# Kernel optimization log

Hardware: AMD Instinct MI355X
Metric: run time of the kernel (lower is better)

The kernel has to match this reference:

```python
import jax, jax.numpy as jnp
import numpy as np

VOCAB, T, E, H, O, B = 401, 140, 128, 256, 3, 4096


def setup_inputs() -> dict:
    key = jax.random.key(0)
    ks = jax.random.split(key, 8)
    s_e = 1.0 / np.sqrt(H)
    return {
        "input": jax.random.randint(ks[0], (B, T), 0, VOCAB),
        "hidden": jnp.zeros((B, H), dtype=jnp.float32),
        "embed": jax.random.normal(ks[1], (VOCAB, E), dtype=jnp.float32),
        "W_ih": jax.random.uniform(ks[2], (3 * H, E), jnp.float32, -s_e, s_e),
        "W_hh": jax.random.uniform(ks[3], (3 * H, H), jnp.float32, -s_e, s_e),
        "b_ih": jax.random.uniform(ks[4], (3 * H,), jnp.float32, -s_e, s_e),
        "b_hh": jax.random.uniform(ks[5], (3 * H,), jnp.float32, -s_e, s_e),
        "W_out": jax.random.uniform(ks[6], (O, H), jnp.float32, -s_e, s_e),
        "b_out": jax.random.uniform(ks[7], (O,), jnp.float32, -s_e, s_e),
    }


def reference(input, hidden, embed, W_ih, W_hh, b_ih, b_hh, W_out, b_out):
    # Embedding lookup: [B, T, E]
    x = embed[input]
    # Precompute input-side gate projections for all timesteps: [B, T, 3H]
    gi = jnp.einsum("bte,ge->btg", x, W_ih) + b_ih

    def step(h, gi_t):
        gh = h @ W_hh.T + b_hh  # [B, 3H]
        i_r, i_z, i_n = jnp.split(gi_t, 3, axis=-1)
        h_r, h_z, h_n = jnp.split(gh, 3, axis=-1)
        r = jax.nn.sigmoid(i_r + h_r)
        z = jax.nn.sigmoid(i_z + h_z)
        n = jnp.tanh(i_n + r * h_n)
        h_new = (1.0 - z) * n + z * h
        return h_new, None

    h_final, _ = jax.lax.scan(step, hidden, jnp.swapaxes(gi, 0, 1))
    logits = h_final @ W_out.T + b_out  # [B, O]
    return jax.nn.log_softmax(logits, axis=1), h_final
```

## Files before the change

kernel.cpp:

```cpp
#include <hip/hip_runtime.h>

typedef __attribute__((ext_vector_type(8))) short short8;
typedef __attribute__((ext_vector_type(4))) float f32x4;
typedef unsigned short ushort_t;
typedef unsigned int uint_t;

#define VOCAB 401
#define T_ 140
#define E_ 128
#define H_ 256
#define B_ 4096
#define HPAD 264

__device__ float Gf[VOCAB * 768];
__device__ ushort_t WhhB[768 * H_];

__device__ __forceinline__ float bf2f(ushort_t u) {
  union { uint_t i; float f; } x; x.i = ((uint_t)u) << 16; return x.f;
}
__device__ __forceinline__ ushort_t f2bf(float f) {
  union { float f; uint_t i; } x; x.f = f;
  uint_t r = x.i + 0x7FFFu + ((x.i >> 16) & 1u);
  return (ushort_t)(r >> 16);
}
__device__ __forceinline__ float fast_sigmoid(float x) {
  return __builtin_amdgcn_rcpf(1.f + __builtin_amdgcn_exp2f(-1.442695041f * x));
}
__device__ __forceinline__ float fast_tanh(float x) {
  return 1.f - 2.f * __builtin_amdgcn_rcpf(1.f + __builtin_amdgcn_exp2f(2.885390082f * x));
}
__device__ __forceinline__ float ldf(const void* p, size_t i, int isb) {
  return isb ? bf2f(((const ushort_t*)p)[i]) : ((const float*)p)[i];
}
__device__ __forceinline__ void ld8f(const void* p, size_t idx, int isb, float* o) {
  if (isb) {
    short8 v = *(const short8*)((const ushort_t*)p + idx);
#pragma unroll
    for (int e = 0; e < 8; ++e) o[e] = bf2f((ushort_t)v[e]);
  } else {
    f32x4 a = *(const f32x4*)((const float*)p + idx);
    f32x4 b = *(const f32x4*)((const float*)p + idx + 4);
#pragma unroll
    for (int e = 0; e < 4; ++e) { o[e] = a[e]; o[4 + e] = b[e]; }
  }
}
__device__ __forceinline__ int block_probe_isbf16(const ushort_t* embed_raw, int* s) {
  if (threadIdx.x < 64) {
    ushort_t v = embed_raw[2 * threadIdx.x];
    int e = (v >> 7) & 0xFF;
    unsigned long long m = __ballot(e >= 100 && e <= 140);
    if (threadIdx.x == 0) *s = (__popcll(m) >= 40) ? 1 : 0;
  }
  __syncthreads();
  return *s;
}

__global__ void canon_whh(const void* __restrict__ W_hh, const ushort_t* __restrict__ embed_raw) {
  __shared__ int sISB;
  int isb = block_probe_isbf16(embed_raw, &sISB);
  int i4 = (blockIdx.x * 256 + threadIdx.x) * 4;
  if (isb) {
    *(uint2*)&WhhB[i4] = *(const uint2*)((const ushort_t*)W_hh + i4);
  } else {
    f32x4 v = *(const f32x4*)((const float*)W_hh + i4);
    uint2 pk;
    pk.x = (uint_t)f2bf(v[0]) | ((uint_t)f2bf(v[1]) << 16);
    pk.y = (uint_t)f2bf(v[2]) | ((uint_t)f2bf(v[3]) << 16);
    *(uint2*)&WhhB[i4] = pk;
  }
}

__global__ void build_G(const void* __restrict__ embed,
                        const void* __restrict__ W_ih,
                        const void* __restrict__ b_ih,
                        const void* __restrict__ b_hh) {
  __shared__ float emb[E_];
  __shared__ int sISB;
  const int isb = block_probe_isbf16((const ushort_t*)embed, &sISB);
  const int v = blockIdx.x, g = blockIdx.y, j = threadIdx.x;
  if (j < E_) emb[j] = ldf(embed, (size_t)v * E_ + j, isb);
  __syncthreads();
  const int row = g * H_ + j;
  float s = 0.f;
#pragma unroll
  for (int k8 = 0; k8 < E_ / 8; ++k8) {
    float wv[8];
    ld8f(W_ih, (size_t)row * E_ + k8 * 8, isb, wv);
#pragma unroll
    for (int e = 0; e < 8; ++e) s += emb[k8 * 8 + e] * wv[e];
  }
  s += ldf(b_ih, row, isb);
  if (g < 2) s += ldf(b_hh, row, isb);
  Gf[v * 768 + row] = s;
}

__launch_bounds__(1024)
__global__ void gru_persist(const int* __restrict__ input,
                            const void* __restrict__ hidden,
                            const void* __restrict__ b_hh,
                            const void* __restrict__ W_out,
                            const void* __restrict__ b_out,
                            const ushort_t* __restrict__ embed_raw,
                            void* __restrict__ out) {
  __shared__ ushort_t hB[2][16 * HPAD];
  __shared__ float bhhn[H_];
  __shared__ int ids[16 * T_];
  __shared__ int sISB;

  const int isb  = block_probe_isbf16(embed_raw, &sISB);
  const int tid  = threadIdx.x;
  const int w    = tid >> 6;
  const int lane = tid & 63;
  const int quad = lane >> 4;
  const int col  = lane & 15;
  const int wg   = blockIdx.x;
  const int u0   = w << 4;
  const int u0q  = u0 + (quad << 2);

  if (tid < 512) {
    int r = tid >> 5, c0 = (tid & 31) << 3;
    size_t gi = (size_t)(wg * 16 + r) * H_ + c0;
    ushort_t* dst = &hB[0][r * HPAD + c0];
    if (isb) {
      *(short8*)dst = *(const short8*)((const ushort_t*)hidden + gi);
    } else {
      float tmp[8];
      ld8f(hidden, gi, 0, tmp);
#pragma unroll
      for (int e = 0; e < 8; ++e) dst[e] = f2bf(tmp[e]);
    }
  }
  if (tid < H_) bhhn[tid] = ldf(b_hh, 512 + tid, isb);
  for (int k = tid; k < 16 * T_; k += 1024)
    ids[k] = input[(size_t)wg * 16 * T_ + k] * 3072;

  short8 wA[3][8];
#pragma unroll
  for (int g = 0; g < 3; ++g) {
    const ushort_t* wrow = WhhB + (size_t)(g * H_ + u0 + col) * H_ + (quad << 3);
#pragma unroll
    for (int kt = 0; kt < 8; ++kt) wA[g][kt] = *(const short8*)(wrow + kt * 32);
  }

  __syncthreads();

  float hreg[4];
#pragma unroll
  for (int i = 0; i < 4; ++i)
    hreg[i] = bf2f(hB[0][col * HPAD + u0q + i]);

  const int idbase = col * T_;
  const char* gB = (const char*)Gf + (size_t)u0q * 4;

  f32x4 accr, accz, gin;
  {
    int goff = ids[idbase];
    accr = *(const f32x4*)(gB + goff);
    accz = *(const f32x4*)(gB + goff + H_ * 4);
    gin  = *(const f32x4*)(gB + goff + 2 * H_ * 4);
  }

  for (int t = 0; t < T_; ++t) {
    const int cur = t & 1;
    const int nxt = cur ^ 1;
    const ushort_t* hr = &hB[cur][col * HPAD + (quad << 3)];

    f32x4 an = {0.f, 0.f, 0.f, 0.f};
#pragma unroll
    for (int kt = 0; kt < 8; ++kt) {
      short8 b = *(const short8*)(hr + kt * 32);
      accr = __builtin_amdgcn_mfma_f32_16x16x32_bf16(wA[0][kt], b, accr, 0, 0, 0);
      accz = __builtin_amdgcn_mfma_f32_16x16x32_bf16(wA[1][kt], b, accz, 0, 0, 0);
      an   = __builtin_amdgcn_mfma_f32_16x16x32_bf16(wA[2][kt], b, an,   0, 0, 0);
    }

    int tn = t + 1; if (tn == T_) tn = 0;
    int goff2 = ids[idbase + tn];

    f32x4 bh = *(const f32x4*)&bhhn[u0q];

    uint_t rr[4];
#pragma unroll
    for (int i = 0; i < 4; ++i) {
      float r_ = fast_sigmoid(accr[i]);
      float z_ = fast_sigmoid(accz[i]);
      float hn = an[i] + bh[i];
      float n  = fast_tanh(gin[i] + r_ * hn);
      float h  = n + z_ * (hreg[i] - n);
      hreg[i] = h;
      union { float f; uint_t u; } c; c.f = h;
      rr[i] = c.u + 0x7FFFu + ((c.u >> 16) & 1u);
    }
    ushort_t* hw = &hB[nxt][col * HPAD + u0q];
    *(uint_t*)&hw[0] = __builtin_amdgcn_perm(rr[1], rr[0], 0x07060302);
    *(uint_t*)&hw[2] = __builtin_amdgcn_perm(rr[3], rr[2], 0x07060302);

    accr = *(const f32x4*)(gB + goff2);
    accz = *(const f32x4*)(gB + goff2 + H_ * 4);
    gin  = *(const f32x4*)(gB + goff2 + 2 * H_ * 4);

    __syncthreads();
  }

  {
    const ushort_t* hrow = &hB[0][w * HPAD + (lane << 2)];
    float h0 = bf2f(hrow[0]), h1 = bf2f(hrow[1]), h2 = bf2f(hrow[2]), h3 = bf2f(hrow[3]);
    float d[3];
#pragma unroll
    for (int o = 0; o < 3; ++o) {
      size_t base = (size_t)o * H_ + (lane << 2);
      d[o] = ldf(W_out, base, isb) * h0 + ldf(W_out, base + 1, isb) * h1 +
             ldf(W_out, base + 2, isb) * h2 + ldf(W_out, base + 3, isb) * h3;
      for (int off = 1; off < 64; off <<= 1) d[o] += __shfl_xor(d[o], off);
    }
    if (lane == 0) {
      float l0 = d[0] + ldf(b_out, 0, isb);
      float l1 = d[1] + ldf(b_out, 1, isb);
      float l2 = d[2] + ldf(b_out, 2, isb);
      float m = fmaxf(l0, fmaxf(l1, l2));
      float s = __builtin_amdgcn_exp2f((l0 - m) * 1.442695041f) +
                __builtin_amdgcn_exp2f((l1 - m) * 1.442695041f) +
                __builtin_amdgcn_exp2f((l2 - m) * 1.442695041f);
      float ls = __builtin_amdgcn_logf(s) * 0.6931471806f;
      size_t ob = (size_t)(wg * 16 + w) * 3;
      float o0 = l0 - m - ls, o1 = l1 - m - ls, o2 = l2 - m - ls;
      if (isb) {
        ushort_t* ob16 = (ushort_t*)out;
        ob16[ob] = f2bf(o0); ob16[ob + 1] = f2bf(o1); ob16[ob + 2] = f2bf(o2);
      } else {
        float* of = (float*)out;
        of[ob] = o0; of[ob + 1] = o1; of[ob + 2] = o2;
      }
    }
  }
  {
    int e = tid << 2;
    int bb = e >> 8, uu = e & 255;
    const ushort_t* src = &hB[0][bb * HPAD + uu];
    size_t oi = 12288 + (size_t)wg * 4096 + e;
    if (isb) {
      *(uint2*)((ushort_t*)out + oi) = *(const uint2*)src;
    } else {
      float* of = (float*)out;
      of[oi] = bf2f(src[0]); of[oi + 1] = bf2f(src[1]);
      of[oi + 2] = bf2f(src[2]); of[oi + 3] = bf2f(src[3]);
    }
  }
}

extern "C" void kernel_launch(void* const* d_in, const int* in_sizes, int n_in,
                              void* d_out, int out_size, void* d_ws, size_t ws_size,
                              hipStream_t stream) {
  (void)in_sizes; (void)n_in; (void)out_size; (void)d_ws; (void)ws_size;
  const int* input = (const int*)d_in[0];
  const void* hidden = d_in[1];
  const void* embed  = d_in[2];
  const void* W_ih   = d_in[3];
  const void* W_hh   = d_in[4];
  const void* b_hh   = d_in[6];
  const void* W_out  = d_in[7];
  const void* b_out  = d_in[8];
  const void* b_ih   = d_in[5];

  canon_whh<<<192, 256, 0, stream>>>(W_hh, (const ushort_t*)embed);
  build_G<<<dim3(VOCAB, 3), 256, 0, stream>>>(embed, W_ih, b_ih, b_hh);
  gru_persist<<<B_ / 16, 1024, 0, stream>>>(input, hidden, b_hh, W_out, b_out,
                                            (const ushort_t*)embed, d_out);
}
```

Baseline: 435.0 us.

## Halve GRU block to 512 threads with two row-tiles per wave

The persistent GRU kernel now runs 8 waves per block, each owning two 16-unit tiles, so weight fragments double per wave. Launch bounds allow two blocks per CU. The n-gate bias is folded into the MFMA accumulator init and the id table is padded to drop the wrap branch. build_G now processes 8 vocab rows per block, reusing each W_ih load across 8 embeddings. Register pressure rises (wA holds 48 short8), which risks spills or lower occupancy.

```diff
diff --git a/kernel.cpp b/kernel.cpp
--- a/kernel.cpp
+++ b/kernel.cpp
@@ -74,27 +74,39 @@
                         const void* __restrict__ W_ih,
                         const void* __restrict__ b_ih,
                         const void* __restrict__ b_hh) {
-  __shared__ float emb[E_];
+  __shared__ float emb[8][E_];
   __shared__ int sISB;
   const int isb = block_probe_isbf16((const ushort_t*)embed, &sISB);
-  const int v = blockIdx.x, g = blockIdx.y, j = threadIdx.x;
-  if (j < E_) emb[j] = ldf(embed, (size_t)v * E_ + j, isb);
+  const int vb = blockIdx.x;
+  const int g  = blockIdx.y;
+  const int j  = threadIdx.x;
+  for (int idx = j; idx < 8 * E_; idx += 256) {
+    int s = idx >> 7, e = idx & 127;
+    int v = vb * 8 + s; if (v > VOCAB - 1) v = VOCAB - 1;
+    emb[s][e] = ldf(embed, (size_t)v * E_ + e, isb);
+  }
   __syncthreads();
   const int row = g * H_ + j;
-  float s = 0.f;
-#pragma unroll
+  float acc[8];
+#pragma unroll
+  for (int s = 0; s < 8; ++s) acc[s] = 0.f;
   for (int k8 = 0; k8 < E_ / 8; ++k8) {
     float wv[8];
     ld8f(W_ih, (size_t)row * E_ + k8 * 8, isb, wv);
 #pragma unroll
-    for (int e = 0; e < 8; ++e) s += emb[k8 * 8 + e] * wv[e];
-  }
-  s += ldf(b_ih, row, isb);
-  if (g < 2) s += ldf(b_hh, row, isb);
-  Gf[v * 768 + row] = s;
-}
-
-__launch_bounds__(1024)
+    for (int s = 0; s < 8; ++s)
+#pragma unroll
+      for (int e = 0; e < 8; ++e) acc[s] += emb[s][k8 * 8 + e] * wv[e];
+  }
+  float bias = ldf(b_ih, row, isb) + ((g < 2) ? ldf(b_hh, row, isb) : 0.f);
+#pragma unroll
+  for (int s = 0; s < 8; ++s) {
+    int v = vb * 8 + s;
+    if (v < VOCAB) Gf[v * 768 + row] = acc[s] + bias;
+  }
+}
+
+__launch_bounds__(512, 2)
 __global__ void gru_persist(const int* __restrict__ input,
                             const void* __restrict__ hidden,
                             const void* __restrict__ b_hh,
@@ -104,7 +116,7 @@
                             void* __restrict__ out) {
   __shared__ ushort_t hB[2][16 * HPAD];
   __shared__ float bhhn[H_];
-  __shared__ int ids[16 * T_];
+  __shared__ int ids[16 * (T_ + 1)];
   __shared__ int sISB;
 
   const int isb  = block_probe_isbf16(embed_raw, &sISB);
@@ -114,10 +126,11 @@
   const int quad = lane >> 4;
   const int col  = lane & 15;
   const int wg   = blockIdx.x;
-  const int u0   = w << 4;
-  const int u0q  = u0 + (quad << 2);
-
-  if (tid < 512) {
+  const int u0   = w << 5;
+  const int u0q0 = u0 + (quad << 2);
+  const int u0q1 = u0 + 16 + (quad << 2);
+
+  {
     int r = tid >> 5, c0 = (tid & 31) << 3;
     size_t gi = (size_t)(wg * 16 + r) * H_ + c0;
     ushort_t* dst = &hB[0][r * HPAD + c0];
@@ -131,79 +144,114 @@
     }
   }
   if (tid < H_) bhhn[tid] = ldf(b_hh, 512 + tid, isb);
-  for (int k = tid; k < 16 * T_; k += 1024)
-    ids[k] = input[(size_t)wg * 16 * T_ + k] * 3072;
-
-  short8 wA[3][8];
-#pragma unroll
-  for (int g = 0; g < 3; ++g) {
-    const ushort_t* wrow = WhhB + (size_t)(g * H_ + u0 + col) * H_ + (quad << 3);
-#pragma unroll
-    for (int kt = 0; kt < 8; ++kt) wA[g][kt] = *(const short8*)(wrow + kt * 32);
-  }
+  for (int k = tid; k < 16 * (T_ + 1); k += 512) {
+    int b = k / (T_ + 1), t = k - b * (T_ + 1);
+    ids[k] = (t < T_) ? input[(size_t)wg * 16 * T_ + b * T_ + t] * 3072 : 0;
+  }
+
+  short8 wA[3][2][8];
+#pragma unroll
+  for (int g = 0; g < 3; ++g)
+#pragma unroll
+    for (int tl = 0; tl < 2; ++tl) {
+      const ushort_t* wrow = WhhB + (size_t)(g * H_ + u0 + tl * 16 + col) * H_ + (quad << 3);
+#pragma unroll
+      for (int kt = 0; kt < 8; ++kt) wA[g][tl][kt] = *(const short8*)(wrow + kt * 32);
+    }
 
   __syncthreads();
 
-  float hreg[4];
-#pragma unroll
-  for (int i = 0; i < 4; ++i)
-    hreg[i] = bf2f(hB[0][col * HPAD + u0q + i]);
-
-  const int idbase = col * T_;
-  const char* gB = (const char*)Gf + (size_t)u0q * 4;
-
-  f32x4 accr, accz, gin;
+  float hreg0[4], hreg1[4];
+#pragma unroll
+  for (int i = 0; i < 4; ++i) {
+    hreg0[i] = bf2f(hB[0][col * HPAD + u0q0 + i]);
+    hreg1[i] = bf2f(hB[0][col * HPAD + u0q1 + i]);
+  }
+  const f32x4 bh0 = *(const f32x4*)&bhhn[u0q0];
+  const f32x4 bh1 = *(const f32x4*)&bhhn[u0q1];
+
+  const int idbase = col * (T_ + 1);
+  const char* gB = (const char*)Gf + (size_t)u0q0 * 4;
+
+  f32x4 a0r, a0z, g0n, a1r, a1z, g1n;
   {
     int goff = ids[idbase];
-    accr = *(const f32x4*)(gB + goff);
-    accz = *(const f32x4*)(gB + goff + H_ * 4);
-    gin  = *(const f32x4*)(gB + goff + 2 * H_ * 4);
-  }
-
+    a0r = *(const f32x4*)(gB + goff);
+    a0z = *(const f32x4*)(gB + goff + 1024);
+    g0n = *(const f32x4*)(gB + goff + 2048);
+    a1r = *(const f32x4*)(gB + goff + 64);
+    a1z = *(const f32x4*)(gB + goff + 1024 + 64);
+    g1n = *(const f32x4*)(gB + goff + 2048 + 64);
+  }
+
+#pragma unroll 2
   for (int t = 0; t < T_; ++t) {
     const int cur = t & 1;
     const int nxt = cur ^ 1;
     const ushort_t* hr = &hB[cur][col * HPAD + (quad << 3)];
-
-    f32x4 an = {0.f, 0.f, 0.f, 0.f};
+    const int goff_n = ids[idbase + t + 1];
+
+    f32x4 a0n = bh0;
 #pragma unroll
     for (int kt = 0; kt < 8; ++kt) {
       short8 b = *(const short8*)(hr + kt * 32);
-      accr = __builtin_amdgcn_mfma_f32_16x16x32_bf16(wA[0][kt], b, accr, 0, 0, 0);
-      accz = __builtin_amdgcn_mfma_f32_16x16x32_bf16(wA[1][kt], b, accz, 0, 0, 0);
-      an   = __builtin_amdgcn_mfma_f32_16x16x32_bf16(wA[2][kt], b, an,   0, 0, 0);
-    }
-
-    int tn = t + 1; if (tn == T_) tn = 0;
-    int goff2 = ids[idbase + tn];
-
-    f32x4 bh = *(const f32x4*)&bhhn[u0q];
-
-    uint_t rr[4];
-#pragma unroll
-    for (int i = 0; i < 4; ++i) {
-      float r_ = fast_sigmoid(accr[i]);
-      float z_ = fast_sigmoid(accz[i]);
-      float hn = an[i] + bh[i];
-      float n  = fast_tanh(gin[i] + r_ * hn);
-      float h  = n + z_ * (hreg[i] - n);
-      hreg[i] = h;
-      union { float f; uint_t u; } c; c.f = h;
-      rr[i] = c.u + 0x7FFFu + ((c.u >> 16) & 1u);
-    }
-    ushort_t* hw = &hB[nxt][col * HPAD + u0q];
-    *(uint_t*)&hw[0] = __builtin_amdgcn_perm(rr[1], rr[0], 0x07060302);
-    *(uint_t*)&hw[2] = __builtin_amdgcn_perm(rr[3], rr[2], 0x07060302);
-
-    accr = *(const f32x4*)(gB + goff2);
-    accz = *(const f32x4*)(gB + goff2 + H_ * 4);
-    gin  = *(const f32x4*)(gB + goff2 + 2 * H_ * 4);
+      a0r = __builtin_amdgcn_mfma_f32_16x16x32_bf16(wA[0][0][kt], b, a0r, 0, 0, 0);
+      a0z = __builtin_amdgcn_mfma_f32_16x16x32_bf16(wA[1][0][kt], b, a0z, 0, 0, 0);
+      a0n = __builtin_amdgcn_mfma_f32_16x16x32_bf16(wA[2][0][kt], b, a0n, 0, 0, 0);
+    }
+    {
+      uint_t rr[4];
+#pragma unroll
+      for (int i = 0; i < 4; ++i) {
+        float r_ = fast_sigmoid(a0r[i]);
+        float z_ = fast_sigmoid(a0z[i]);
+        float n  = fast_tanh(g0n[i] + r_ * a0n[i]);
+        float h  = n + z_ * (hreg0[i] - n);
+        hreg0[i] = h;
+        union { float f; uint_t u; } c; c.f = h;
+        rr[i] = c.u + 0x7FFFu + ((c.u >> 16) & 1u);
+      }
+      ushort_t* hw = &hB[nxt][col * HPAD + u0q0];
+      *(uint_t*)&hw[0] = __builtin_amdgcn_perm(rr[1], rr[0], 0x07060302);
+      *(uint_t*)&hw[2] = __builtin_amdgcn_perm(rr[3], rr[2], 0x07060302);
+    }
+    a0r = *(const f32x4*)(gB + goff_n);
+    a0z = *(const f32x4*)(gB + goff_n + 1024);
+    g0n = *(const f32x4*)(gB + goff_n + 2048);
+
+    f32x4 a1n = bh1;
+#pragma unroll
+    for (int kt = 0; kt < 8; ++kt) {
+      short8 b = *(const short8*)(hr + kt * 32);
+      a1r = __builtin_amdgcn_mfma_f32_16x16x32_bf16(wA[0][1][kt], b, a1r, 0, 0, 0);
+      a1z = __builtin_amdgcn_mfma_f32_16x16x32_bf16(wA[1][1][kt], b, a1z, 0, 0, 0);
+      a1n = __builtin_amdgcn_mfma_f32_16x16x32_bf16(wA[2][1][kt], b, a1n, 0, 0, 0);
+    }
+    {
+      uint_t rr[4];
+#pragma unroll
+      for (int i = 0; i < 4; ++i) {
+        float r_ = fast_sigmoid(a1r[i]);
+        float z_ = fast_sigmoid(a1z[i]);
+        float n  = fast_tanh(g1n[i] + r_ * a1n[i]);
+        float h  = n + z_ * (hreg1[i] - n);
+        hreg1[i] = h;
+        union { float f; uint_t u; } c; c.f = h;
+        rr[i] = c.u + 0x7FFFu + ((c.u >> 16) & 1u);
+      }
+      ushort_t* hw = &hB[nxt][col * HPAD + u0q1];
+      *(uint_t*)&hw[0] = __builtin_amdgcn_perm(rr[1], rr[0], 0x07060302);
+      *(uint_t*)&hw[2] = __builtin_amdgcn_perm(rr[3], rr[2], 0x07060302);
+    }
+    a1r = *(const f32x4*)(gB + goff_n + 64);
+    a1z = *(const f32x4*)(gB + goff_n + 1024 + 64);
+    g1n = *(const f32x4*)(gB + goff_n + 2048 + 64);
 
     __syncthreads();
   }
 
-  {
-    const ushort_t* hrow = &hB[0][w * HPAD + (lane << 2)];
+  for (int rb = w; rb < 16; rb += 8) {
+    const ushort_t* hrow = &hB[0][rb * HPAD + (lane << 2)];
     float h0 = bf2f(hrow[0]), h1 = bf2f(hrow[1]), h2 = bf2f(hrow[2]), h3 = bf2f(hrow[3]);
     float d[3];
 #pragma unroll
@@ -222,7 +270,7 @@
                 __builtin_amdgcn_exp2f((l1 - m) * 1.442695041f) +
                 __builtin_amdgcn_exp2f((l2 - m) * 1.442695041f);
       float ls = __builtin_amdgcn_logf(s) * 0.6931471806f;
-      size_t ob = (size_t)(wg * 16 + w) * 3;
+      size_t ob = (size_t)(wg * 16 + rb) * 3;
       float o0 = l0 - m - ls, o1 = l1 - m - ls, o2 = l2 - m - ls;
       if (isb) {
         ushort_t* ob16 = (ushort_t*)out;
@@ -234,16 +282,16 @@
     }
   }
   {
-    int e = tid << 2;
+    int e = tid << 3;
     int bb = e >> 8, uu = e & 255;
     const ushort_t* src = &hB[0][bb * HPAD + uu];
     size_t oi = 12288 + (size_t)wg * 4096 + e;
     if (isb) {
-      *(uint2*)((ushort_t*)out + oi) = *(const uint2*)src;
+      *(short8*)((ushort_t*)out + oi) = *(const short8*)src;
     } else {
       float* of = (float*)out;
-      of[oi] = bf2f(src[0]); of[oi + 1] = bf2f(src[1]);
-      of[oi + 2] = bf2f(src[2]); of[oi + 3] = bf2f(src[3]);
+#pragma unroll
+      for (int q = 0; q < 8; ++q) of[oi + q] = bf2f(src[q]);
     }
   }
 }
@@ -257,13 +305,13 @@
   const void* embed  = d_in[2];
   const void* W_ih   = d_in[3];
   const void* W_hh   = d_in[4];
+  const void* b_ih   = d_in[5];
   const void* b_hh   = d_in[6];
   const void* W_out  = d_in[7];
   const void* b_out  = d_in[8];
-  const void* b_ih   = d_in[5];
 
   canon_whh<<<192, 256, 0, stream>>>(W_hh, (const ushort_t*)embed);
-  build_G<<<dim3(VOCAB, 3), 256, 0, stream>>>(embed, W_ih, b_ih, b_hh);
-  gru_persist<<<B_ / 16, 1024, 0, stream>>>(input, hidden, b_hh, W_out, b_out,
-                                            (const ushort_t*)embed, d_out);
-}
+  build_G<<<dim3(51, 3), 256, 0, stream>>>(embed, W_ih, b_ih, b_hh);
+  gru_persist<<<B_ / 16, 512, 0, stream>>>(input, hidden, b_hh, W_out, b_out,
+                                           (const ushort_t*)embed, d_out);
+}
```

Measured after the change: 443.7 us. +2.0%, slower.

## Merge prep kernels, interleave sigmoid with n-gate MFMAs, use raw barrier

Applied to the files above, without the earlier changes.

The two setup kernels become one launch. The input-projection table build now handles 8 vocab rows per block, so each W_ih load is reused across those rows. In the recurrent loop, the n-gate MFMA chain now runs after r/z, with the sigmoid math interleaved and b_hh_n folded into the accumulator init. The ids table gets a padded sentinel column so the next-step index needs no wrap check, and __syncthreads is replaced by an explicit lgkmcnt wait plus s_barrier. The aim is to hide the transcendental latency behind matrix work and cut per-step sync and launch overhead, at the cost of relying on hand-placed barrier semantics.

```diff
diff --git a/kernel.cpp b/kernel.cpp
--- a/kernel.cpp
+++ b/kernel.cpp
@@ -55,43 +55,57 @@
   return *s;
 }
 
-__global__ void canon_whh(const void* __restrict__ W_hh, const ushort_t* __restrict__ embed_raw) {
-  __shared__ int sISB;
-  int isb = block_probe_isbf16(embed_raw, &sISB);
-  int i4 = (blockIdx.x * 256 + threadIdx.x) * 4;
-  if (isb) {
-    *(uint2*)&WhhB[i4] = *(const uint2*)((const ushort_t*)W_hh + i4);
-  } else {
-    f32x4 v = *(const f32x4*)((const float*)W_hh + i4);
-    uint2 pk;
-    pk.x = (uint_t)f2bf(v[0]) | ((uint_t)f2bf(v[1]) << 16);
-    pk.y = (uint_t)f2bf(v[2]) | ((uint_t)f2bf(v[3]) << 16);
-    *(uint2*)&WhhB[i4] = pk;
-  }
-}
-
-__global__ void build_G(const void* __restrict__ embed,
-                        const void* __restrict__ W_ih,
-                        const void* __restrict__ b_ih,
-                        const void* __restrict__ b_hh) {
-  __shared__ float emb[E_];
+__global__ void prep(const void* __restrict__ W_hh,
+                     const void* __restrict__ embed,
+                     const void* __restrict__ W_ih,
+                     const void* __restrict__ b_ih,
+                     const void* __restrict__ b_hh) {
+  __shared__ float emb[8][E_];
   __shared__ int sISB;
   const int isb = block_probe_isbf16((const ushort_t*)embed, &sISB);
-  const int v = blockIdx.x, g = blockIdx.y, j = threadIdx.x;
-  if (j < E_) emb[j] = ldf(embed, (size_t)v * E_ + j, isb);
+  const int bid = blockIdx.x;
+  const int j = threadIdx.x;
+
+  if (bid >= 153) {
+    int i4 = ((bid - 153) * 256 + j) * 4;
+    if (isb) {
+      *(uint2*)&WhhB[i4] = *(const uint2*)((const ushort_t*)W_hh + i4);
+    } else {
+      f32x4 v = *(const f32x4*)((const float*)W_hh + i4);
+      uint2 pk;
+      pk.x = (uint_t)f2bf(v[0]) | ((uint_t)f2bf(v[1]) << 16);
+      pk.y = (uint_t)f2bf(v[2]) | ((uint_t)f2bf(v[3]) << 16);
+      *(uint2*)&WhhB[i4] = pk;
+    }
+    return;
+  }
+
+  const int vb = bid / 3;
+  const int g  = bid - vb * 3;
+  for (int idx = j; idx < 8 * E_; idx += 256) {
+    int s = idx >> 7, e = idx & 127;
+    int v = vb * 8 + s; if (v > VOCAB - 1) v = VOCAB - 1;
+    emb[s][e] = ldf(embed, (size_t)v * E_ + e, isb);
+  }
   __syncthreads();
   const int row = g * H_ + j;
-  float s = 0.f;
-#pragma unroll
+  float acc[8];
+#pragma unroll
+  for (int s = 0; s < 8; ++s) acc[s] = 0.f;
   for (int k8 = 0; k8 < E_ / 8; ++k8) {
     float wv[8];
     ld8f(W_ih, (size_t)row * E_ + k8 * 8, isb, wv);
 #pragma unroll
-    for (int e = 0; e < 8; ++e) s += emb[k8 * 8 + e] * wv[e];
-  }
-  s += ldf(b_ih, row, isb);
-  if (g < 2) s += ldf(b_hh, row, isb);
-  Gf[v * 768 + row] = s;
+    for (int s = 0; s < 8; ++s)
+#pragma unroll
+      for (int e = 0; e < 8; ++e) acc[s] += emb[s][k8 * 8 + e] * wv[e];
+  }
+  float bias = ldf(b_ih, row, isb) + ((g < 2) ? ldf(b_hh, row, isb) : 0.f);
+#pragma unroll
+  for (int s = 0; s < 8; ++s) {
+    int v = vb * 8 + s;
+    if (v < VOCAB) Gf[v * 768 + row] = acc[s] + bias;
+  }
 }
 
 __launch_bounds__(1024)
@@ -104,7 +118,7 @@
                             void* __restrict__ out) {
   __shared__ ushort_t hB[2][16 * HPAD];
   __shared__ float bhhn[H_];
-  __shared__ int ids[16 * T_];
+  __shared__ int ids[16 * (T_ + 1)];
   __shared__ int sISB;
 
   const int isb  = block_probe_isbf16(embed_raw, &sISB);
@@ -131,8 +145,10 @@
     }
   }
   if (tid < H_) bhhn[tid] = ldf(b_hh, 512 + tid, isb);
-  for (int k = tid; k < 16 * T_; k += 1024)
-    ids[k] = input[(size_t)wg * 16 * T_ + k] * 3072;
+  for (int k = tid; k < 16 * (T_ + 1); k += 1024) {
+    int b = k / (T_ + 1), t = k - b * (T_ + 1);
+    ids[k] = (t < T_) ? input[(size_t)wg * 16 * T_ + b * T_ + t] * 3072 : 0;
+  }
 
   short8 wA[3][8];
 #pragma unroll
@@ -149,44 +165,46 @@
   for (int i = 0; i < 4; ++i)
     hreg[i] = bf2f(hB[0][col * HPAD + u0q + i]);
 
-  const int idbase = col * T_;
+  const int idbase = col * (T_ + 1);
   const char* gB = (const char*)Gf + (size_t)u0q * 4;
 
   f32x4 accr, accz, gin;
   {
     int goff = ids[idbase];
     accr = *(const f32x4*)(gB + goff);
-    accz = *(const f32x4*)(gB + goff + H_ * 4);
-    gin  = *(const f32x4*)(gB + goff + 2 * H_ * 4);
-  }
-
+    accz = *(const f32x4*)(gB + goff + 1024);
+    gin  = *(const f32x4*)(gB + goff + 2048);
+  }
+
+#pragma unroll 2
   for (int t = 0; t < T_; ++t) {
     const int cur = t & 1;
     const int nxt = cur ^ 1;
     const ushort_t* hr = &hB[cur][col * HPAD + (quad << 3)];
-
-    f32x4 an = {0.f, 0.f, 0.f, 0.f};
+    const int goff_n = ids[idbase + t + 1];
+    f32x4 bhv = *(const f32x4*)&bhhn[u0q];
+
 #pragma unroll
     for (int kt = 0; kt < 8; ++kt) {
       short8 b = *(const short8*)(hr + kt * 32);
       accr = __builtin_amdgcn_mfma_f32_16x16x32_bf16(wA[0][kt], b, accr, 0, 0, 0);
       accz = __builtin_amdgcn_mfma_f32_16x16x32_bf16(wA[1][kt], b, accz, 0, 0, 0);
-      an   = __builtin_amdgcn_mfma_f32_16x16x32_bf16(wA[2][kt], b, an,   0, 0, 0);
-    }
-
-    int tn = t + 1; if (tn == T_) tn = 0;
-    int goff2 = ids[idbase + tn];
-
-    f32x4 bh = *(const f32x4*)&bhhn[u0q];
+    }
+    f32x4 an = bhv;
+    float r_[4], z_[4];
+#pragma unroll
+    for (int kt = 0; kt < 8; ++kt) {
+      short8 b = *(const short8*)(hr + kt * 32);
+      an = __builtin_amdgcn_mfma_f32_16x16x32_bf16(wA[2][kt], b, an, 0, 0, 0);
+      if (kt < 4) r_[kt] = fast_sigmoid(accr[kt]);
+      else        z_[kt - 4] = fast_sigmoid(accz[kt - 4]);
+    }
 
     uint_t rr[4];
 #pragma unroll
     for (int i = 0; i < 4; ++i) {
-      float r_ = fast_sigmoid(accr[i]);
-      float z_ = fast_sigmoid(accz[i]);
-      float hn = an[i] + bh[i];
-      float n  = fast_tanh(gin[i] + r_ * hn);
-      float h  = n + z_ * (hreg[i] - n);
+      float n = fast_tanh(gin[i] + r_[i] * an[i]);
+      float h = n + z_[i] * (hreg[i] - n);
       hreg[i] = h;
       union { float f; uint_t u; } c; c.f = h;
       rr[i] = c.u + 0x7FFFu + ((c.u >> 16) & 1u);
@@ -195,11 +213,11 @@
     *(uint_t*)&hw[0] = __builtin_amdgcn_perm(rr[1], rr[0], 0x07060302);
     *(uint_t*)&hw[2] = __builtin_amdgcn_perm(rr[3], rr[2], 0x07060302);
 
-    accr = *(const f32x4*)(gB + goff2);
-    accz = *(const f32x4*)(gB + goff2 + H_ * 4);
-    gin  = *(const f32x4*)(gB + goff2 + 2 * H_ * 4);
-
-    __syncthreads();
+    accr = *(const f32x4*)(gB + goff_n);
+    accz = *(const f32x4*)(gB + goff_n + 1024);
+    gin  = *(const f32x4*)(gB + goff_n + 2048);
+
+    asm volatile("s_waitcnt lgkmcnt(0)\n\ts_barrier" ::: "memory");
   }
 
   {
@@ -257,13 +275,12 @@
   const void* embed  = d_in[2];
   const void* W_ih   = d_in[3];
   const void* W_hh   = d_in[4];
+  const void* b_ih   = d_in[5];
   const void* b_hh   = d_in[6];
   const void* W_out  = d_in[7];
   const void* b_out  = d_in[8];
-  const void* b_ih   = d_in[5];
-
-  canon_whh<<<192, 256, 0, stream>>>(W_hh, (const ushort_t*)embed);
-  build_G<<<dim3(VOCAB, 3), 256, 0, stream>>>(embed, W_ih, b_ih, b_hh);
+
+  prep<<<345, 256, 0, stream>>>(W_hh, embed, W_ih, b_ih, b_hh);
   gru_persist<<<B_ / 16, 1024, 0, stream>>>(input, hidden, b_hh, W_out, b_out,
                                             (const ushort_t*)embed, d_out);
 }
```

Measured after the change: 363.6 us. 1.2x faster.
